# Kernel tuning notes

Measured on AMD Instinct MI355X. Metric: run time of the kernel, lower is better.

## Reference

```python
import jax, jax.numpy as jnp
import numpy as np

H = 4  # num_heads in every nn.MultiheadAttention


def _mha_self(x, mask, w_in, b_in, w_out, b_out):
    # x: [N, L, E], mask: [N, L] (1 = valid). Matches torch nn.MultiheadAttention
    # self-attention with key_padding_mask, dropout=0 (eval).
    N, L, E = x.shape
    d = E // H
    qkv = x @ w_in.T + b_in                      # [N, L, 3E]
    q, k, v = jnp.split(qkv, 3, axis=-1)
    q = q.reshape(N, L, H, d)
    k = k.reshape(N, L, H, d)
    v = v.reshape(N, L, H, d)
    scale = 1.0 / float(np.sqrt(d))
    scores = jnp.einsum('nlhd,nmhd->nhlm', q, k) * scale
    scores = jnp.where(mask[:, None, None, :] > 0, scores, jnp.float32(-1e9))
    a = jax.nn.softmax(scores, axis=-1)
    o = jnp.einsum('nhlm,nmhd->nlhd', a, v).reshape(N, L, E)
    return o @ w_out.T + b_out


def _mha_cross_seq(q_x, kv_x, w_in, b_in, w_out, b_out):
    # torch MHA called with [B,1,E] tensors (batch_first=False): sequence length = B.
    E = q_x.shape[-1]
    d = E // H
    wq, wk, wv = jnp.split(w_in, 3, axis=0)
    bq, bk, bv = jnp.split(b_in, 3, axis=0)
    q = (q_x @ wq.T + bq).reshape(-1, H, d)
    k = (kv_x @ wk.T + bk).reshape(-1, H, d)
    v = (kv_x @ wv.T + bv).reshape(-1, H, d)
    scale = 1.0 / float(np.sqrt(d))
    a = jax.nn.softmax(jnp.einsum('lhd,mhd->hlm', q, k) * scale, axis=-1)
    o = jnp.einsum('hlm,mhd->lhd', a, v).reshape(-1, E)
    return o @ w_out.T + b_out


def _masked_mean(x, m):
    # (attn_out * mask).sum / (mask.sum + 1e-10); yields 0 for fully-masked rows,
    # matching the torch zero-embedding branches.
    return (x * m[..., None]).sum(axis=1) / (m.sum(axis=1, keepdims=True) + 1e-10)


def _ln(x, g, b, eps=1e-5):
    mu = x.mean(-1, keepdims=True)
    var = ((x - mu) ** 2).mean(-1, keepdims=True)
    return (x - mu) / jnp.sqrt(var + eps) * g + b


def setup_inputs():
    key = jax.random.key(0)
    ks = iter(jax.random.split(key, 48))
    B, S, T, W, E = 8, 8, 16, 64, 768
    F, FD = 20, 256

    def rnd(shape, scale):
        return jax.random.normal(next(ks), shape, jnp.float32) * scale

    inp = {}
    inp['word_embeddings'] = rnd((B, S, T, W, E), 1.0)
    inp['attention_mask'] = jax.random.randint(next(ks), (B, S, T, W), 0, 2, jnp.int32)
    inp['handcrafted_features'] = rnd((B, F), 1.0)
    for name in ('word', 'sent', 'sec'):
        inp[name + '_w_in'] = rnd((3 * E, E), 1.0 / np.sqrt(E))
        inp[name + '_b_in'] = jnp.zeros((3 * E,), jnp.float32)
        inp[name + '_w_out'] = rnd((E, E), 1.0 / np.sqrt(E))
        inp[name + '_b_out'] = jnp.zeros((E,), jnp.float32)
    inp['bp_w'] = rnd((FD, E), 1.0 / np.sqrt(E)); inp['bp_b'] = jnp.zeros((FD,), jnp.float32)
    inp['hp_w'] = rnd((FD, F), 1.0 / np.sqrt(F)); inp['hp_b'] = jnp.zeros((FD,), jnp.float32)
    inp['fa_w_in'] = rnd((3 * FD, FD), 1.0 / np.sqrt(FD)); inp['fa_b_in'] = jnp.zeros((3 * FD,), jnp.float32)
    inp['fa_w_out'] = rnd((FD, FD), 1.0 / np.sqrt(FD)); inp['fa_b_out'] = jnp.zeros((FD,), jnp.float32)
    inp['gate_w'] = rnd((FD, 2 * FD), 1.0 / np.sqrt(2 * FD)); inp['gate_b'] = jnp.zeros((FD,), jnp.float32)
    inp['fus_ln_g'] = jnp.ones((FD,), jnp.float32); inp['fus_ln_b'] = jnp.zeros((FD,), jnp.float32)
    inp['fc1_w'] = rnd((128, FD), 1.0 / np.sqrt(FD)); inp['fc1_b'] = jnp.zeros((128,), jnp.float32)
    inp['ln1_g'] = jnp.ones((128,), jnp.float32); inp['ln1_b'] = jnp.zeros((128,), jnp.float32)
    inp['fc2_w'] = rnd((3, 128), 1.0 / np.sqrt(128)); inp['fc2_b'] = jnp.zeros((3,), jnp.float32)
    return inp


def reference(word_embeddings, attention_mask, handcrafted_features,
              word_w_in, word_b_in, word_w_out, word_b_out,
              sent_w_in, sent_b_in, sent_w_out, sent_b_out,
              sec_w_in, sec_b_in, sec_w_out, sec_b_out,
              bp_w, bp_b, hp_w, hp_b,
              fa_w_in, fa_b_in, fa_w_out, fa_b_out,
              gate_w, gate_b, fus_ln_g, fus_ln_b,
              fc1_w, fc1_b, ln1_g, ln1_b, fc2_w, fc2_b):
    B, S, T, W, E = word_embeddings.shape
    m = attention_mask.astype(jnp.float32)
    # word-level attention over all B*S*T sentences at once
    x = word_embeddings.reshape(B * S * T, W, E)
    mw = m.reshape(B * S * T, W)
    wo = _mha_self(x, mw, word_w_in, word_b_in, word_w_out, word_b_out)
    sent = _masked_mean(wo, mw).reshape(B * S, T, E)        # sentence embeddings
    # sentence-level attention per section
    ms = (m.sum(-1) > 0).astype(jnp.float32).reshape(B * S, T)
    so = _mha_self(sent, ms, sent_w_in, sent_b_in, sent_w_out, sent_b_out)
    sec = _masked_mean(so, ms).reshape(B, S, E)             # section embeddings
    # section-level attention per document
    msec = (m.sum((-1, -2)) > 0).astype(jnp.float32)        # [B, S]
    do = _mha_self(sec, msec, sec_w_in, sec_b_in, sec_w_out, sec_b_out)
    doc = _masked_mean(do, msec)                            # [B, E]
    # feature fusion (the cross-attention output is computed but unused downstream,
    # exactly as in the torch code)
    bert_proj = doc @ bp_w.T + bp_b                         # [B, 256]
    hand_proj = handcrafted_features @ hp_w.T + hp_b        # [B, 256]
    _ = _mha_cross_seq(bert_proj, hand_proj, fa_w_in, fa_b_in, fa_w_out, fa_b_out)
    gate = jax.nn.sigmoid(jnp.concatenate([bert_proj, hand_proj], -1) @ gate_w.T + gate_b)
    fused = gate * bert_proj + (1.0 - gate) * hand_proj
    fused = _ln(fused, fus_ln_g, fus_ln_b)                  # dropout = identity (eval)
    h1 = jax.nn.relu(fused @ fc1_w.T + fc1_b)
    h1 = _ln(h1, ln1_g, ln1_b)
    return h1 @ fc2_w.T + fc2_b                             # [B, num_classes]
```

## Files before the change

### kernel.cpp

```cpp
#include <hip/hip_runtime.h>
#include <math.h>

#define EDIM 768
#define E3 2304
#define NT8 24

typedef __attribute__((ext_vector_type(8))) short short8;
typedef __attribute__((ext_vector_type(8))) unsigned short ushort8;
typedef __attribute__((ext_vector_type(4))) float f32x4;

__device__ inline void gload_lds16(const void* g, void* l) {
  __builtin_amdgcn_global_load_lds((const __attribute__((address_space(1))) void*)g,
                                   (__attribute__((address_space(3))) void*)l, 16, 0, 0);
}

__device__ inline unsigned short f2b_rne(float f) {
  unsigned int u = __builtin_bit_cast(unsigned int, f);
  u = (u + 0x7fffu + ((u >> 16) & 1u)) >> 16;
  return (unsigned short)u;
}
__device__ inline float b2f(unsigned short u) {
  unsigned int x = ((unsigned int)u) << 16;
  return __builtin_bit_cast(float, x);
}
__device__ inline float ldv(float v) { return v; }
__device__ inline float ldv(unsigned short v) { return b2f(v); }

__global__ __launch_bounds__(256) void f2bf(const float* __restrict__ in,
                                            unsigned short* __restrict__ out, size_t n) {
  size_t i = ((size_t)blockIdx.x * blockDim.x + threadIdx.x) * 8;
  size_t stride = (size_t)gridDim.x * blockDim.x * 8;
  for (; i < n; i += stride) {
    float4 a = *(const float4*)(in + i);
    float4 b = *(const float4*)(in + i + 4);
    ushort8 o;
    o[0] = f2b_rne(a.x); o[1] = f2b_rne(a.y); o[2] = f2b_rne(a.z); o[3] = f2b_rne(a.w);
    o[4] = f2b_rne(b.x); o[5] = f2b_rne(b.y); o[6] = f2b_rne(b.z); o[7] = f2b_rne(b.w);
    *(ushort8*)(out + i) = o;
  }
}

__global__ void mask_stats1(const int* __restrict__ am, float* __restrict__ wsum,
                            float* __restrict__ svalid) {
  int n = blockIdx.x * blockDim.x + threadIdx.x;
  if (n < 1024) {
    int s = 0;
    const int* p = am + (size_t)n * 64;
    for (int w = 0; w < 64; ++w) s += p[w];
    wsum[n] = (float)s;
    svalid[n] = s > 0 ? 1.f : 0.f;
  }
}

__global__ void mask_stats2(const float* __restrict__ wsum, const float* __restrict__ svalid,
                            float* __restrict__ cnt2, float* __restrict__ secv,
                            float* __restrict__ cnt3) {
  int tid = threadIdx.x;
  if (tid < 64) {
    float c = 0.f, t = 0.f;
    for (int u = 0; u < 16; ++u) { c += svalid[tid * 16 + u]; t += wsum[tid * 16 + u]; }
    cnt2[tid] = c;
    secv[tid] = t > 0.f ? 1.f : 0.f;
  }
  __syncthreads();
  if (tid < 8) {
    float c = 0.f;
    for (int s = 0; s < 8; ++s) c += secv[tid * 8 + s];
    cnt3[tid] = c;
  }
}

__global__ __launch_bounds__(512, 2) void gemm8(
    const unsigned short* __restrict__ A, const unsigned short* __restrict__ B,
    const float* __restrict__ bias, unsigned short* __restrict__ C,
    int M, int N, int K) {
  __shared__ unsigned short lds[4][2][8192];
  const int tid = threadIdx.x;
  const int w = tid >> 6;
  const int lane = tid & 63;
  const int nbx = N / 256;
  const int nwg = gridDim.x;
  const int cpx = nwg >> 3;
  const int bid = blockIdx.x;
  const int swz = (bid & 7) * cpx + (bid >> 3);
  const int m0 = (swz / nbx) * 256;
  const int n0 = (swz % nbx) * 256;
  const int wr = w >> 2, wc = w & 3;
  const int fr = lane & 15;
  const int g = lane >> 4;
  f32x4 acc[8][4] = {};

  int srow[2], scol[2];
#pragma unroll
  for (int q = 0; q < 2; ++q) {
    int S = q * 512 + tid;
    int row = S >> 2;
    srow[q] = row;
    scol[q] = ((S & 3) ^ ((row >> 1) & 3)) * 8;
  }
  auto stageA = [&](int t) {
    const int kt = t * 32;
#pragma unroll
    for (int q = 0; q < 2; ++q)
      gload_lds16(A + (size_t)(m0 + srow[q]) * K + kt + scol[q],
                  &lds[t & 3][0][(q * 8 + w) * 512]);
  };
  auto stageB = [&](int t) {
    const int kt = t * 32;
#pragma unroll
    for (int q = 0; q < 2; ++q)
      gload_lds16(B + (size_t)(n0 + srow[q]) * K + kt + scol[q],
                  &lds[t & 3][1][(q * 8 + w) * 512]);
  };
  int aoff[8], boff[4];
#pragma unroll
  for (int i = 0; i < 8; ++i) {
    int r = wr * 128 + i * 16 + fr;
    aoff[i] = (r * 4 + (g ^ ((r >> 1) & 3))) * 8;
  }
#pragma unroll
  for (int j = 0; j < 4; ++j) {
    int r = wc * 64 + j * 16 + fr;
    boff[j] = (r * 4 + (g ^ ((r >> 1) & 3))) * 8;
  }

  stageA(0); stageB(0); stageA(1); stageB(1); stageA(2); stageB(2);
  asm volatile("s_waitcnt vmcnt(8)" ::: "memory");
  __builtin_amdgcn_sched_barrier(0);
  __builtin_amdgcn_s_barrier();
  __builtin_amdgcn_sched_barrier(0);

  for (int t = 0; t < NT8; ++t) {
    const unsigned short* la = lds[t & 3][0];
    const unsigned short* lb = lds[t & 3][1];
    short8 av[8], bv0, bv1;
#pragma unroll
    for (int i = 0; i < 8; ++i) av[i] = *(const short8*)(la + aoff[i]);
    bv0 = *(const short8*)(lb + boff[0]);
    bv1 = *(const short8*)(lb + boff[1]);
    if (t + 3 < NT8) stageA(t + 3);
    __builtin_amdgcn_sched_barrier(0);
    __builtin_amdgcn_s_barrier();
    __builtin_amdgcn_sched_barrier(0);
    __builtin_amdgcn_s_setprio(1);
#pragma unroll
    for (int i = 0; i < 8; ++i) {
      acc[i][0] = __builtin_amdgcn_mfma_f32_16x16x32_bf16(av[i], bv0, acc[i][0], 0, 0, 0);
      acc[i][1] = __builtin_amdgcn_mfma_f32_16x16x32_bf16(av[i], bv1, acc[i][1], 0, 0, 0);
    }
    __builtin_amdgcn_s_setprio(0);
    __builtin_amdgcn_sched_barrier(0);
    __builtin_amdgcn_s_barrier();
    __builtin_amdgcn_sched_barrier(0);
    bv0 = *(const short8*)(lb + boff[2]);
    bv1 = *(const short8*)(lb + boff[3]);
    if (t + 3 < NT8) stageB(t + 3);
    __builtin_amdgcn_sched_barrier(0);
    __builtin_amdgcn_s_barrier();
    __builtin_amdgcn_sched_barrier(0);
    __builtin_amdgcn_s_setprio(1);
#pragma unroll
    for (int i = 0; i < 8; ++i) {
      acc[i][2] = __builtin_amdgcn_mfma_f32_16x16x32_bf16(av[i], bv0, acc[i][2], 0, 0, 0);
      acc[i][3] = __builtin_amdgcn_mfma_f32_16x16x32_bf16(av[i], bv1, acc[i][3], 0, 0, 0);
    }
    __builtin_amdgcn_s_setprio(0);
    if (t < NT8 - 3) {
      asm volatile("s_waitcnt vmcnt(8)" ::: "memory");
    } else if (t == NT8 - 3) {
      asm volatile("s_waitcnt vmcnt(4)" ::: "memory");
    } else {
      asm volatile("s_waitcnt vmcnt(0)" ::: "memory");
    }
    __builtin_amdgcn_sched_barrier(0);
    __builtin_amdgcn_s_barrier();
    __builtin_amdgcn_sched_barrier(0);
  }

  const int cl = lane & 15;
  const int rg = (lane >> 4) * 4;
#pragma unroll
  for (int i = 0; i < 8; ++i) {
    const int mrow0 = m0 + wr * 128 + i * 16 + rg;
#pragma unroll
    for (int j = 0; j < 4; ++j) {
      const int col = n0 + wc * 64 + j * 16 + cl;
      const float bvv = bias[col];
#pragma unroll
      for (int r = 0; r < 4; ++r)
        C[(size_t)(mrow0 + r) * N + col] = f2b_rne(acc[i][j][r] + bvv);
    }
  }
}

__global__ __launch_bounds__(256) void attn_qk(
    const unsigned short* __restrict__ qk, const unsigned short* __restrict__ xbf,
    const int* __restrict__ am, const float* __restrict__ wsum,
    unsigned short* __restrict__ xbarbf) {
  __shared__ float abar_all[4][64];
  __shared__ float msk[64];
  const int n = blockIdx.x;
  const int tid = threadIdx.x;
  const int h = tid >> 6;
  const int lane = tid & 63;
  if (tid < 64) msk[tid] = (am[(size_t)n * 64 + tid] > 0) ? 1.f : 0.f;
  __syncthreads();
  const int fr = lane & 15;
  const int fk = (lane >> 4) * 8;
  const unsigned short* Qg = qk + (size_t)n * 64 * 1536 + h * 192;
  const unsigned short* Kg = Qg + 768;
  f32x4 acc[4][4] = {};
#pragma unroll
  for (int ks = 0; ks < 6; ++ks) {
    short8 aq[4], bk[4];
#pragma unroll
    for (int i = 0; i < 4; ++i)
      aq[i] = *(const short8*)(Qg + (size_t)(i * 16 + fr) * 1536 + ks * 32 + fk);
#pragma unroll
    for (int j = 0; j < 4; ++j)
      bk[j] = *(const short8*)(Kg + (size_t)(j * 16 + fr) * 1536 + ks * 32 + fk);
#pragma unroll
    for (int i = 0; i < 4; ++i)
#pragma unroll
      for (int j = 0; j < 4; ++j)
        acc[i][j] = __builtin_amdgcn_mfma_f32_16x16x32_bf16(aq[i], bk[j], acc[i][j], 0, 0, 0);
  }
  const float den = wsum[n] + 1e-10f;
  const float scale = 0.07216878364870323f;
  float mcol[4];
#pragma unroll
  for (int j = 0; j < 4; ++j) mcol[j] = msk[j * 16 + fr];
  float colsum[4] = {0.f, 0.f, 0.f, 0.f};
#pragma unroll
  for (int i = 0; i < 4; ++i) {
#pragma unroll
    for (int r = 0; r < 4; ++r) {
      float s[4];
      float mx = -1e30f;
#pragma unroll
      for (int j = 0; j < 4; ++j) {
        float v = mcol[j] > 0.f ? acc[i][j][r] * scale : -1e9f;
        s[j] = v;
        mx = fmaxf(mx, v);
      }
      mx = fmaxf(mx, __shfl_xor(mx, 1));
      mx = fmaxf(mx, __shfl_xor(mx, 2));
      mx = fmaxf(mx, __shfl_xor(mx, 4));
      mx = fmaxf(mx, __shfl_xor(mx, 8));
      float sum = 0.f;
#pragma unroll
      for (int j = 0; j < 4; ++j) { s[j] = expf(s[j] - mx); sum += s[j]; }
      sum += __shfl_xor(sum, 1);
      sum += __shfl_xor(sum, 2);
      sum += __shfl_xor(sum, 4);
      sum += __shfl_xor(sum, 8);
      float wrow = msk[i * 16 + (lane >> 4) * 4 + r] / den;
      float f = wrow / sum;
#pragma unroll
      for (int j = 0; j < 4; ++j) colsum[j] += s[j] * f;
    }
  }
#pragma unroll
  for (int j = 0; j < 4; ++j) {
    float cs = colsum[j];
    cs += __shfl_xor(cs, 16);
    cs += __shfl_xor(cs, 32);
    if (lane < 16) abar_all[h][j * 16 + lane] = cs;
  }
  __syncthreads();
  const unsigned short* xg = xbf + (size_t)n * 64 * 768;
  float a4[4][3] = {};
  for (int m = 0; m < 64; ++m) {
    float ab0 = abar_all[0][m], ab1 = abar_all[1][m];
    float ab2 = abar_all[2][m], ab3 = abar_all[3][m];
#pragma unroll
    for (int u = 0; u < 3; ++u) {
      float x = b2f(xg[(size_t)m * 768 + u * 256 + tid]);
      a4[0][u] += ab0 * x;
      a4[1][u] += ab1 * x;
      a4[2][u] += ab2 * x;
      a4[3][u] += ab3 * x;
    }
  }
#pragma unroll
  for (int hh = 0; hh < 4; ++hh)
#pragma unroll
    for (int u = 0; u < 3; ++u)
      xbarbf[((size_t)hh * 1024 + n) * 768 + u * 256 + tid] = f2b_rne(a4[hh][u]);
}

__global__ __launch_bounds__(256) void gemm_bf16_64(
    const unsigned short* __restrict__ A, const unsigned short* __restrict__ B,
    const float* __restrict__ bias, const float* __restrict__ cnt,
    float* __restrict__ C, unsigned short* __restrict__ Cb,
    int K, int ldc, size_t Az, size_t Bz, int colz) {
  __shared__ unsigned short smA[128 * 32];
  __shared__ unsigned short smB[64 * 32];
  const int tid = threadIdx.x;
  const int wid = tid >> 6;
  const int lane = tid & 63;
  const int za = blockIdx.z;
  A += (size_t)za * Az;
  B += (size_t)za * Bz;
  const int m0 = blockIdx.y * 128;
  const int nb = blockIdx.x * 64;
  const int wr = wid >> 1, wc = wid & 1;
  const int srow = lane >> 2;
  const int scol = (lane & 3) * 8;
  const int fr = lane & 15;
  const int fk = (lane >> 4) * 8;
  f32x4 acc[4][2] = {};
  for (int k0 = 0; k0 < K; k0 += 32) {
#pragma unroll
    for (int t = 0; t < 2; ++t) {
      const int r0 = wid * 32 + t * 16;
      gload_lds16(A + (size_t)(m0 + r0 + srow) * K + k0 + scol, &smA[r0 * 32]);
    }
    gload_lds16(B + (size_t)(nb + wid * 16 + srow) * K + k0 + scol, &smB[wid * 16 * 32]);
    __syncthreads();
    short8 af[4], bfr[2];
#pragma unroll
    for (int i = 0; i < 4; ++i)
      af[i] = *(const short8*)&smA[(wr * 64 + i * 16 + fr) * 32 + fk];
#pragma unroll
    for (int j = 0; j < 2; ++j)
      bfr[j] = *(const short8*)&smB[(wc * 32 + j * 16 + fr) * 32 + fk];
#pragma unroll
    for (int i = 0; i < 4; ++i)
#pragma unroll
      for (int j = 0; j < 2; ++j)
        acc[i][j] = __builtin_amdgcn_mfma_f32_16x16x32_bf16(af[i], bfr[j], acc[i][j], 0, 0, 0);
    __syncthreads();
  }
  const int cl = lane & 15;
  const int rg = (lane >> 4) * 4;
#pragma unroll
  for (int i = 0; i < 4; ++i) {
    const int mrow0 = m0 + wr * 64 + i * 16 + rg;
#pragma unroll
    for (int j = 0; j < 2; ++j) {
      const int gc = za * colz + nb + wc * 32 + j * 16 + cl;
      const float bv = bias[gc];
#pragma unroll
      for (int r = 0; r < 4; ++r) {
        const int m = mrow0 + r;
        float sf = 1.f;
        if (cnt) { float c = cnt[m]; sf = c / (c + 1e-10f); }
        float v = acc[i][j][r] + bv * sf;
        if (Cb) Cb[(size_t)m * ldc + gc] = f2b_rne(v);
        else C[(size_t)m * ldc + gc] = v;
      }
    }
  }
}

#define BM 64
#define BN 64
#define BK 16
__global__ __launch_bounds__(256) void gemm_nt(
    const float* __restrict__ X, const float* __restrict__ W,
    const float* __restrict__ bias, const float* __restrict__ cnt,
    float* __restrict__ out, int M, int N, int K, int lda, int ldc) {
  __shared__ float As[BK][BM + 4];
  __shared__ float Bs[BK][BN + 4];
  const int tid = threadIdx.x;
  const int m0 = blockIdx.y * BM;
  const int n0 = blockIdx.x * BN;
  const int tx = tid & 15, ty = tid >> 4;
  const int lr = tid >> 2;
  const int lc = (tid & 3) * 4;
  float acc[4][4];
#pragma unroll
  for (int i = 0; i < 4; ++i)
#pragma unroll
    for (int j = 0; j < 4; ++j) acc[i][j] = 0.f;
  for (int k0 = 0; k0 < K; k0 += BK) {
    float4 xa = make_float4(0.f, 0.f, 0.f, 0.f);
    if (m0 + lr < M) xa = *(const float4*)(X + (size_t)(m0 + lr) * lda + k0 + lc);
    float4 wb = *(const float4*)(W + (size_t)(n0 + lr) * K + k0 + lc);
    As[lc + 0][lr] = xa.x; As[lc + 1][lr] = xa.y; As[lc + 2][lr] = xa.z; As[lc + 3][lr] = xa.w;
    Bs[lc + 0][lr] = wb.x; Bs[lc + 1][lr] = wb.y; Bs[lc + 2][lr] = wb.z; Bs[lc + 3][lr] = wb.w;
    __syncthreads();
#pragma unroll
    for (int kk = 0; kk < BK; ++kk) {
      float4 av = *(const float4*)&As[kk][ty * 4];
      float4 bv = *(const float4*)&Bs[kk][tx * 4];
      float a4[4] = {av.x, av.y, av.z, av.w};
      float b4[4] = {bv.x, bv.y, bv.z, bv.w};
#pragma unroll
      for (int i = 0; i < 4; ++i)
#pragma unroll
        for (int j = 0; j < 4; ++j) acc[i][j] += a4[i] * b4[j];
    }
    __syncthreads();
  }
#pragma unroll
  for (int i = 0; i < 4; ++i) {
    int m = m0 + ty * 4 + i;
    if (m < M) {
      float sf = 1.f;
      if (cnt) { float c = cnt[m]; sf = c / (c + 1e-10f); }
      float4 o;
      o.x = acc[i][0] + bias[n0 + tx * 4 + 0] * sf;
      o.y = acc[i][1] + bias[n0 + tx * 4 + 1] * sf;
      o.z = acc[i][2] + bias[n0 + tx * 4 + 2] * sf;
      o.w = acc[i][3] + bias[n0 + tx * 4 + 3] * sf;
      *(float4*)(out + (size_t)m * ldc + n0 + tx * 4) = o;
    }
  }
}

template <class T>
__global__ __launch_bounds__(256) void small_attn(
    const T* __restrict__ qkv, const float* __restrict__ maskv,
    const float* __restrict__ cnt, float* __restrict__ obar, int L) {
  const int n = blockIdx.x;
  const int h = blockIdx.y;
  const int tid = threadIdx.x;
  __shared__ float red[16][17];
  __shared__ float abar[16];
  const T* qb = qkv + (size_t)n * L * E3 + h * 192;
  const T* kb = qb + EDIM;
  const T* vb = qb + 2 * EDIM;
  const float scale = 0.07216878364870323f;
  if (tid < L * L) {
    int l = tid / L, m = tid % L;
    float s = 0.f;
    for (int dd = 0; dd < 192; ++dd) s += ldv(qb[(size_t)l * E3 + dd]) * ldv(kb[(size_t)m * E3 + dd]);
    s = (maskv[n * L + m] > 0.f) ? s * scale : -1e9f;
    float mx = s;
    for (int off = L >> 1; off > 0; off >>= 1) mx = fmaxf(mx, __shfl_xor(mx, off));
    float p = expf(s - mx);
    float sum = p;
    for (int off = L >> 1; off > 0; off >>= 1) sum += __shfl_xor(sum, off);
    float dn = cnt[n] + 1e-10f;
    float wl = (maskv[n * L + l] > 0.f) ? (1.f / dn) : 0.f;
    red[l][m] = p / sum * wl;
  }
  __syncthreads();
  if (tid < L) {
    float s = 0.f;
    for (int l2 = 0; l2 < L; ++l2) s += red[l2][tid];
    abar[tid] = s;
  }
  __syncthreads();
  if (tid < 192) {
    float acc = 0.f;
    for (int m = 0; m < L; ++m) acc += abar[m] * ldv(vb[(size_t)m * E3 + tid]);
    obar[(size_t)n * EDIM + h * 192 + tid] = acc;
  }
}

__global__ __launch_bounds__(256) void head_kernel(
    const float* __restrict__ doc, const float* __restrict__ hand,
    const float* __restrict__ bp_w, const float* __restrict__ bp_b,
    const float* __restrict__ hp_w, const float* __restrict__ hp_b,
    const float* __restrict__ gate_w, const float* __restrict__ gate_b,
    const float* __restrict__ fg, const float* __restrict__ fbv,
    const float* __restrict__ fc1_w, const float* __restrict__ fc1_b,
    const float* __restrict__ g1, const float* __restrict__ b1,
    const float* __restrict__ fc2_w, const float* __restrict__ fc2_b,
    float* __restrict__ out) {
  int b = blockIdx.x, tid = threadIdx.x;
  __shared__ float bp[256], hp[256], fz[256], hz[128];
  const float* dr = doc + (size_t)b * 768;
  float acc = bp_b[tid];
  for (int k = 0; k < 768; ++k) acc += dr[k] * bp_w[(size_t)tid * 768 + k];
  bp[tid] = acc;
  const float* hr = hand + b * 20;
  float acc2 = hp_b[tid];
  for (int k = 0; k < 20; ++k) acc2 += hr[k] * hp_w[tid * 20 + k];
  hp[tid] = acc2;
  __syncthreads();
  float g = gate_b[tid];
  for (int k = 0; k < 256; ++k) g += bp[k] * gate_w[tid * 512 + k];
  for (int k = 0; k < 256; ++k) g += hp[k] * gate_w[tid * 512 + 256 + k];
  g = 1.f / (1.f + expf(-g));
  float fu = g * bp[tid] + (1.f - g) * hp[tid];
  fz[tid] = fu;
  __syncthreads();
  float mu = 0.f;
  for (int k = 0; k < 256; ++k) mu += fz[k];
  mu /= 256.f;
  float va = 0.f;
  for (int k = 0; k < 256; ++k) { float d = fz[k] - mu; va += d * d; }
  va /= 256.f;
  float fl = (fu - mu) / sqrtf(va + 1e-5f) * fg[tid] + fbv[tid];
  __syncthreads();
  fz[tid] = fl;
  __syncthreads();
  if (tid < 128) {
    float a = fc1_b[tid];
    for (int k = 0; k < 256; ++k) a += fz[k] * fc1_w[tid * 256 + k];
    hz[tid] = fmaxf(a, 0.f);
  }
  __syncthreads();
  float mu2 = 0.f;
  for (int k = 0; k < 128; ++k) mu2 += hz[k];
  mu2 /= 128.f;
  float va2 = 0.f;
  for (int k = 0; k < 128; ++k) { float d = hz[k] - mu2; va2 += d * d; }
  va2 /= 128.f;
  __syncthreads();
  if (tid < 128) hz[tid] = (hz[tid] - mu2) / sqrtf(va2 + 1e-5f) * g1[tid] + b1[tid];
  __syncthreads();
  if (tid < 3) {
    float o = fc2_b[tid];
    for (int k = 0; k < 128; ++k) o += hz[k] * fc2_w[tid * 128 + k];
    out[b * 3 + tid] = o;
  }
}

extern "C" void kernel_launch(void* const* d_in, const int* in_sizes, int n_in,
                              void* d_out, int out_size, void* d_ws, size_t ws_size,
                              hipStream_t stream) {
  const float* we      = (const float*)d_in[0];
  const int*   am      = (const int*)d_in[1];
  const float* hand    = (const float*)d_in[2];
  const float* w_w_in  = (const float*)d_in[3];
  const float* w_b_in  = (const float*)d_in[4];
  const float* w_w_out = (const float*)d_in[5];
  const float* w_b_out = (const float*)d_in[6];
  const float* s_w_in  = (const float*)d_in[7];
  const float* s_b_in  = (const float*)d_in[8];
  const float* s_w_out = (const float*)d_in[9];
  const float* s_b_out = (const float*)d_in[10];
  const float* c_w_in  = (const float*)d_in[11];
  const float* c_b_in  = (const float*)d_in[12];
  const float* c_w_out = (const float*)d_in[13];
  const float* c_b_out = (const float*)d_in[14];
  const float* bp_w = (const float*)d_in[15];
  const float* bp_b = (const float*)d_in[16];
  const float* hp_w = (const float*)d_in[17];
  const float* hp_b = (const float*)d_in[18];
  const float* gate_w = (const float*)d_in[23];
  const float* gate_b = (const float*)d_in[24];
  const float* fus_g  = (const float*)d_in[25];
  const float* fus_b  = (const float*)d_in[26];
  const float* fc1_w  = (const float*)d_in[27];
  const float* fc1_b  = (const float*)d_in[28];
  const float* ln1_g  = (const float*)d_in[29];
  const float* ln1_b  = (const float*)d_in[30];
  const float* fc2_w  = (const float*)d_in[31];
  const float* fc2_b  = (const float*)d_in[32];
  float* out = (float*)d_out;

  unsigned short* qk  = (unsigned short*)d_ws;
  unsigned short* xbf = qk + (size_t)65536 * 1536;

  char* end = (char*)d_ws + ws_size;
  auto carveb = [&](size_t bytes) {
    size_t b = (bytes + 255) & ~(size_t)255;
    end -= b;
    return (void*)end;
  };
  unsigned short* xbarbf  = (unsigned short*)carveb((size_t)4 * 1024 * 768 * 2);
  unsigned short* obarbf  = (unsigned short*)carveb((size_t)1024 * 768 * 2);
  unsigned short* sentbf  = (unsigned short*)carveb((size_t)1024 * 768 * 2);
  unsigned short* qkv2bf  = (unsigned short*)carveb((size_t)1024 * 2304 * 2);
  float* obar2  = (float*)carveb(64 * 768 * 4);
  float* sec    = (float*)carveb(64 * 768 * 4);
  float* qkv3   = (float*)carveb(64 * 2304 * 4);
  float* obar3  = (float*)carveb(8 * 768 * 4);
  float* doc    = (float*)carveb(8 * 768 * 4);
  float* wsum   = (float*)carveb(1024 * 4);
  float* svalid = (float*)carveb(1024 * 4);
  float* cnt2   = (float*)carveb(64 * 4);
  float* secv   = (float*)carveb(64 * 4);
  float* cnt3   = (float*)carveb(8 * 4);
  unsigned short* wbf_in = (unsigned short*)carveb((size_t)2304 * 768 * 2);
  unsigned short* wobf   = (unsigned short*)carveb((size_t)768 * 768 * 2);
  unsigned short* wsbf   = (unsigned short*)carveb((size_t)2304 * 768 * 2);

  auto cgrid = [](size_t n) { size_t g = (n + 2047) / 2048; return (int)(g > 2048 ? 2048 : g); };

  f2bf<<<cgrid((size_t)2304 * 768), 256, 0, stream>>>(w_w_in, wbf_in, (size_t)2304 * 768);
  f2bf<<<cgrid((size_t)768 * 768), 256, 0, stream>>>(w_w_out, wobf, (size_t)768 * 768);
  f2bf<<<cgrid((size_t)2304 * 768), 256, 0, stream>>>(s_w_in, wsbf, (size_t)2304 * 768);
  mask_stats1<<<4, 256, 0, stream>>>(am, wsum, svalid);
  mask_stats2<<<1, 64, 0, stream>>>(wsum, svalid, cnt2, secv, cnt3);

  f2bf<<<2048, 256, 0, stream>>>(we, xbf, (size_t)65536 * 768);
  gemm8<<<(65536 / 256) * (1536 / 256), 512, 0, stream>>>(xbf, wbf_in, w_b_in, qk,
                                                          65536, 1536, 768);
  attn_qk<<<1024, 256, 0, stream>>>(qk, xbf, am, wsum, xbarbf);
  gemm_bf16_64<<<dim3(3, 8, 4), 256, 0, stream>>>(
      xbarbf, wbf_in + (size_t)1536 * 768, w_b_in + 1536, wsum, nullptr, obarbf,
      768, 768, (size_t)1024 * 768, (size_t)192 * 768, 192);
  gemm_bf16_64<<<dim3(12, 8, 1), 256, 0, stream>>>(
      obarbf, wobf, w_b_out, wsum, nullptr, sentbf, 768, 768, 0, 0, 0);
  gemm_bf16_64<<<dim3(36, 8, 1), 256, 0, stream>>>(
      sentbf, wsbf, s_b_in, nullptr, nullptr, qkv2bf, 768, 2304, 0, 0, 0);
  small_attn<<<dim3(64, 4), 256, 0, stream>>>(qkv2bf, svalid, cnt2, obar2, 16);
  gemm_nt<<<dim3(12, 1), 256, 0, stream>>>(obar2, s_w_out, s_b_out, cnt2, sec,
                                           64, 768, 768, 768, 768);
  gemm_nt<<<dim3(36, 1), 256, 0, stream>>>(sec, c_w_in, c_b_in, nullptr, qkv3,
                                           64, 2304, 768, 768, 2304);
  small_attn<<<dim3(8, 4), 256, 0, stream>>>(qkv3, secv, cnt3, obar3, 8);
  gemm_nt<<<dim3(12, 1), 256, 0, stream>>>(obar3, c_w_out, c_b_out, cnt3, doc,
                                           8, 768, 768, 768, 768);
  head_kernel<<<8, 256, 0, stream>>>(doc, hand, bp_w, bp_b, hp_w, hp_b, gate_w, gate_b,
                                     fus_g, fus_b, fc1_w, fc1_b, ln1_g, ln1_b, fc2_w, fc2_b, out);
}
```

Baseline: 602.5 us.

## Restructure big QK GEMM to double-buffered K=64 tiles and fuse weight casts

The main 65536x1536x768 GEMM moves from a 4-deep ring of K=32 stages to a 2-slot double buffer of K=64 tiles, using an 8-way XOR swizzle and a single barrier per tile instead of three. The intent is to cut barrier and waitcnt overhead and issue larger MFMA bursts per synchronisation. Prefetch depth drops to one tile and the loop waits for all loads (vmcnt(0)) every iteration, which may expose memory latency. Separately, the three weight fp32-to-bf16 casts are merged into one launch to save launch overhead.

Result: faster. 582.1 us (-3.4%).

```diff
diff --git a/kernel.cpp b/kernel.cpp
--- a/kernel.cpp
+++ b/kernel.cpp
@@ -3,7 +3,6 @@
 
 #define EDIM 768
 #define E3 2304
-#define NT8 24
 
 typedef __attribute__((ext_vector_type(8))) short short8;
 typedef __attribute__((ext_vector_type(8))) unsigned short ushort8;
@@ -40,6 +39,27 @@
   }
 }
 
+__global__ __launch_bounds__(256) void f2bf3(
+    const float* __restrict__ i0, unsigned short* __restrict__ o0, size_t n0,
+    const float* __restrict__ i1, unsigned short* __restrict__ o1, size_t n1,
+    const float* __restrict__ i2, unsigned short* __restrict__ o2, size_t n2) {
+  size_t c8 = (size_t)blockIdx.x * blockDim.x + threadIdx.x;
+  size_t stride = (size_t)gridDim.x * blockDim.x;
+  size_t t0 = n0 >> 3, t1 = t0 + (n1 >> 3), t2 = t1 + (n2 >> 3);
+  for (; c8 < t2; c8 += stride) {
+    const float* src; unsigned short* dst; size_t i;
+    if (c8 < t0) { src = i0; dst = o0; i = c8 * 8; }
+    else if (c8 < t1) { src = i1; dst = o1; i = (c8 - t0) * 8; }
+    else { src = i2; dst = o2; i = (c8 - t1) * 8; }
+    float4 a = *(const float4*)(src + i);
+    float4 b = *(const float4*)(src + i + 4);
+    ushort8 o;
+    o[0] = f2b_rne(a.x); o[1] = f2b_rne(a.y); o[2] = f2b_rne(a.z); o[3] = f2b_rne(a.w);
+    o[4] = f2b_rne(b.x); o[5] = f2b_rne(b.y); o[6] = f2b_rne(b.z); o[7] = f2b_rne(b.w);
+    *(ushort8*)(dst + i) = o;
+  }
+}
+
 __global__ void mask_stats1(const int* __restrict__ am, float* __restrict__ wsum,
                             float* __restrict__ svalid) {
   int n = blockIdx.x * blockDim.x + threadIdx.x;
@@ -74,13 +94,12 @@
     const unsigned short* __restrict__ A, const unsigned short* __restrict__ B,
     const float* __restrict__ bias, unsigned short* __restrict__ C,
     int M, int N, int K) {
-  __shared__ unsigned short lds[4][2][8192];
+  __shared__ unsigned short lds[2][32768];
   const int tid = threadIdx.x;
   const int w = tid >> 6;
   const int lane = tid & 63;
   const int nbx = N / 256;
-  const int nwg = gridDim.x;
-  const int cpx = nwg >> 3;
+  const int cpx = gridDim.x >> 3;
   const int bid = blockIdx.x;
   const int swz = (bid & 7) * cpx + (bid >> 3);
   const int m0 = (swz / nbx) * 256;
@@ -88,93 +107,85 @@
   const int wr = w >> 2, wc = w & 3;
   const int fr = lane & 15;
   const int g = lane >> 4;
+  const int NT64 = K / 64;
   f32x4 acc[8][4] = {};
 
-  int srow[2], scol[2];
-#pragma unroll
-  for (int q = 0; q < 2; ++q) {
+  int srow[4], scol[4];
+#pragma unroll
+  for (int q = 0; q < 4; ++q) {
     int S = q * 512 + tid;
-    int row = S >> 2;
-    srow[q] = row;
-    scol[q] = ((S & 3) ^ ((row >> 1) & 3)) * 8;
-  }
-  auto stageA = [&](int t) {
-    const int kt = t * 32;
-#pragma unroll
-    for (int q = 0; q < 2; ++q)
+    srow[q] = S >> 3;
+    scol[q] = ((S & 7) ^ (srow[q] & 7)) * 8;
+  }
+  auto stageA = [&](int t, int slot) {
+    const int kt = t * 64;
+#pragma unroll
+    for (int q = 0; q < 4; ++q)
       gload_lds16(A + (size_t)(m0 + srow[q]) * K + kt + scol[q],
-                  &lds[t & 3][0][(q * 8 + w) * 512]);
+                  &lds[slot][(q * 512 + w * 64) * 8]);
   };
-  auto stageB = [&](int t) {
-    const int kt = t * 32;
-#pragma unroll
-    for (int q = 0; q < 2; ++q)
+  auto stageB = [&](int t, int slot) {
+    const int kt = t * 64;
+#pragma unroll
+    for (int q = 0; q < 4; ++q)
       gload_lds16(B + (size_t)(n0 + srow[q]) * K + kt + scol[q],
-                  &lds[t & 3][1][(q * 8 + w) * 512]);
+                  &lds[slot][16384 + (q * 512 + w * 64) * 8]);
   };
-  int aoff[8], boff[4];
-#pragma unroll
-  for (int i = 0; i < 8; ++i) {
-    int r = wr * 128 + i * 16 + fr;
-    aoff[i] = (r * 4 + (g ^ ((r >> 1) & 3))) * 8;
-  }
-#pragma unroll
-  for (int j = 0; j < 4; ++j) {
-    int r = wc * 64 + j * 16 + fr;
-    boff[j] = (r * 4 + (g ^ ((r >> 1) & 3))) * 8;
-  }
-
-  stageA(0); stageB(0); stageA(1); stageB(1); stageA(2); stageB(2);
-  asm volatile("s_waitcnt vmcnt(8)" ::: "memory");
+  int aoff[2][8], boff[2][4];
+#pragma unroll
+  for (int ks = 0; ks < 2; ++ks) {
+#pragma unroll
+    for (int i = 0; i < 8; ++i) {
+      int r = wr * 128 + i * 16 + fr;
+      aoff[ks][i] = (r * 8 + ((ks * 4 + g) ^ (r & 7))) * 8;
+    }
+#pragma unroll
+    for (int j = 0; j < 4; ++j) {
+      int r = wc * 64 + j * 16 + fr;
+      boff[ks][j] = 16384 + (r * 8 + ((ks * 4 + g) ^ (r & 7))) * 8;
+    }
+  }
+
+  stageA(0, 0);
+  stageB(0, 0);
+  asm volatile("s_waitcnt vmcnt(0)" ::: "memory");
   __builtin_amdgcn_sched_barrier(0);
   __builtin_amdgcn_s_barrier();
   __builtin_amdgcn_sched_barrier(0);
 
-  for (int t = 0; t < NT8; ++t) {
-    const unsigned short* la = lds[t & 3][0];
-    const unsigned short* lb = lds[t & 3][1];
-    short8 av[8], bv0, bv1;
-#pragma unroll
-    for (int i = 0; i < 8; ++i) av[i] = *(const short8*)(la + aoff[i]);
-    bv0 = *(const short8*)(lb + boff[0]);
-    bv1 = *(const short8*)(lb + boff[1]);
-    if (t + 3 < NT8) stageA(t + 3);
+  int slot = 0;
+  for (int t = 0; t < NT64; ++t) {
+    const unsigned short* ls = lds[slot];
+    if (t + 1 < NT64) stageA(t + 1, slot ^ 1);
+    short8 av[8], bv[4];
+#pragma unroll
+    for (int i = 0; i < 8; ++i) av[i] = *(const short8*)(ls + aoff[0][i]);
+#pragma unroll
+    for (int j = 0; j < 4; ++j) bv[j] = *(const short8*)(ls + boff[0][j]);
+    __builtin_amdgcn_s_setprio(1);
+#pragma unroll
+    for (int i = 0; i < 8; ++i)
+#pragma unroll
+      for (int j = 0; j < 4; ++j)
+        acc[i][j] = __builtin_amdgcn_mfma_f32_16x16x32_bf16(av[i], bv[j], acc[i][j], 0, 0, 0);
+    __builtin_amdgcn_s_setprio(0);
+    if (t + 1 < NT64) stageB(t + 1, slot ^ 1);
+#pragma unroll
+    for (int i = 0; i < 8; ++i) av[i] = *(const short8*)(ls + aoff[1][i]);
+#pragma unroll
+    for (int j = 0; j < 4; ++j) bv[j] = *(const short8*)(ls + boff[1][j]);
+    __builtin_amdgcn_s_setprio(1);
+#pragma unroll
+    for (int i = 0; i < 8; ++i)
+#pragma unroll
+      for (int j = 0; j < 4; ++j)
+        acc[i][j] = __builtin_amdgcn_mfma_f32_16x16x32_bf16(av[i], bv[j], acc[i][j], 0, 0, 0);
+    __builtin_amdgcn_s_setprio(0);
+    asm volatile("s_waitcnt vmcnt(0)" ::: "memory");
     __builtin_amdgcn_sched_barrier(0);
     __builtin_amdgcn_s_barrier();
     __builtin_amdgcn_sched_barrier(0);
-    __builtin_amdgcn_s_setprio(1);
-#pragma unroll
-    for (int i = 0; i < 8; ++i) {
-      acc[i][0] = __builtin_amdgcn_mfma_f32_16x16x32_bf16(av[i], bv0, acc[i][0], 0, 0, 0);
-      acc[i][1] = __builtin_amdgcn_mfma_f32_16x16x32_bf16(av[i], bv1, acc[i][1], 0, 0, 0);
-    }
-    __builtin_amdgcn_s_setprio(0);
-    __builtin_amdgcn_sched_barrier(0);
-    __builtin_amdgcn_s_barrier();
-    __builtin_amdgcn_sched_barrier(0);
-    bv0 = *(const short8*)(lb + boff[2]);
-    bv1 = *(const short8*)(lb + boff[3]);
-    if (t + 3 < NT8) stageB(t + 3);
-    __builtin_amdgcn_sched_barrier(0);
-    __builtin_amdgcn_s_barrier();
-    __builtin_amdgcn_sched_barrier(0);
-    __builtin_amdgcn_s_setprio(1);
-#pragma unroll
-    for (int i = 0; i < 8; ++i) {
-      acc[i][2] = __builtin_amdgcn_mfma_f32_16x16x32_bf16(av[i], bv0, acc[i][2], 0, 0, 0);
-      acc[i][3] = __builtin_amdgcn_mfma_f32_16x16x32_bf16(av[i], bv1, acc[i][3], 0, 0, 0);
-    }
-    __builtin_amdgcn_s_setprio(0);
-    if (t < NT8 - 3) {
-      asm volatile("s_waitcnt vmcnt(8)" ::: "memory");
-    } else if (t == NT8 - 3) {
-      asm volatile("s_waitcnt vmcnt(4)" ::: "memory");
-    } else {
-      asm volatile("s_waitcnt vmcnt(0)" ::: "memory");
-    }
-    __builtin_amdgcn_sched_barrier(0);
-    __builtin_amdgcn_s_barrier();
-    __builtin_amdgcn_sched_barrier(0);
+    slot ^= 1;
   }
 
   const int cl = lane & 15;
@@ -572,11 +583,9 @@
   unsigned short* wobf   = (unsigned short*)carveb((size_t)768 * 768 * 2);
   unsigned short* wsbf   = (unsigned short*)carveb((size_t)2304 * 768 * 2);
 
-  auto cgrid = [](size_t n) { size_t g = (n + 2047) / 2048; return (int)(g > 2048 ? 2048 : g); };
-
-  f2bf<<<cgrid((size_t)2304 * 768), 256, 0, stream>>>(w_w_in, wbf_in, (size_t)2304 * 768);
-  f2bf<<<cgrid((size_t)768 * 768), 256, 0, stream>>>(w_w_out, wobf, (size_t)768 * 768);
-  f2bf<<<cgrid((size_t)2304 * 768), 256, 0, stream>>>(s_w_in, wsbf, (size_t)2304 * 768);
+  f2bf3<<<2048, 256, 0, stream>>>(w_w_in, wbf_in, (size_t)2304 * 768,
+                                  w_w_out, wobf, (size_t)768 * 768,
+                                  s_w_in, wsbf, (size_t)2304 * 768);
   mask_stats1<<<4, 256, 0, stream>>>(am, wsum, svalid);
   mask_stats2<<<1, 64, 0, stream>>>(wsum, svalid, cnt2, secv, cnt3);
 
```
